# Optimization experiments

Hardware: AMD Instinct MI355X
Metric: run time of the kernel (lower is better)

Reference implementation:

```python
import jax, jax.numpy as jnp
import numpy as np

N = 50000     # nodes
E = 800000    # edges (before self-loops)
DIN = 128     # input feature dim
DH = 16       # per-head hidden dim (layer 1)
H = 8         # heads (layer 1)
DOUT = 64     # output classes (layer 2, heads=1)


def setup_inputs() -> dict:
    key = jax.random.key(0)
    ks = jax.random.split(key, 10)
    def rn(k, shape, scale=0.1):
        return jax.random.normal(k, shape, dtype=jnp.float32) * scale
    x = jax.random.normal(ks[0], (N, DIN), dtype=jnp.float32)
    edge_index = jax.random.randint(ks[1], (2, E), 0, N, dtype=jnp.int64)
    return {
        "x": x,
        "edge_index": edge_index,
        "W1": rn(ks[2], (DIN, H * DH)),
        "a_src1": rn(ks[3], (H, DH)),
        "a_dst1": rn(ks[4], (H, DH)),
        "b1": jnp.zeros((H * DH,), jnp.float32),
        "W2": rn(ks[5], (H * DH, DOUT)),
        "a_src2": rn(ks[6], (1, DOUT)),
        "a_dst2": rn(ks[7], (1, DOUT)),
        "b2": jnp.zeros((DOUT,), jnp.float32),
    }


def gat_conv(x, src, dst, W, a_src, a_dst, b, heads, out_dim):
    """PyG-style GATConv: edge attention + segment softmax over dst + scatter-add."""
    n = x.shape[0]
    h = (x @ W).reshape(n, heads, out_dim)                 # [N, H, D]
    alpha_src = jnp.sum(h * a_src, axis=-1)                # [N, H]
    alpha_dst = jnp.sum(h * a_dst, axis=-1)                # [N, H]
    e = jax.nn.leaky_relu(alpha_src[src] + alpha_dst[dst], 0.2)  # [Etot, H]
    # numerically-stable segment softmax grouped by destination node
    m = jax.ops.segment_max(e, dst, num_segments=n)        # [N, H]
    ex = jnp.exp(e - m[dst])
    s = jax.ops.segment_sum(ex, dst, num_segments=n)       # [N, H]
    alpha = ex / (s[dst] + 1e-16)                          # [Etot, H]
    msg = h[src] * alpha[..., None]                        # [Etot, H, D]
    out = jax.ops.segment_sum(msg, dst, num_segments=n)    # [N, H, D]
    return out.reshape(n, heads * out_dim) + b


def reference(x, W1, a_src1, a_dst1, b1, W2, a_src2, a_dst2, b2, edge_index):
    # eval mode: F.dropout(p=0.6, training=False) is identity
    loop = jnp.arange(N, dtype=edge_index.dtype)
    src = jnp.concatenate([edge_index[0], loop])  # add_self_loops=True (PyG default)
    dst = jnp.concatenate([edge_index[1], loop])
    h = gat_conv(x, src, dst, W1, a_src1, a_dst1, b1, H, DH)
    h = jax.nn.elu(h)
    h = gat_conv(h, src, dst, W2, a_src2, a_dst2, b2, 1, DOUT)
    return (h, jax.nn.log_softmax(h, axis=1))
```

## Files before the change

### kernel.cpp

```cpp
#include <hip/hip_runtime.h>

#define NN 50000
#define EE 800000
#define ET (EE + NN)

typedef unsigned short ushort_t;

__device__ __forceinline__ float bf2f(ushort_t u) {
    return __uint_as_float(((unsigned int)u) << 16);
}
__device__ __forceinline__ ushort_t f2bf(float f) {
    unsigned int u = __float_as_uint(f);
    u += 0x7fffu + ((u >> 16) & 1u);
    return (ushort_t)(u >> 16);
}
__device__ __forceinline__ float lrelu(float e) {
    return fmaxf(e, 0.f) + 0.2f * fminf(e, 0.f);
}
__device__ __forceinline__ float ldf(const void* p, int i, bool f32) {
    return f32 ? ((const float*)p)[i] : bf2f(((const ushort_t*)p)[i]);
}

__global__ __launch_bounds__(256) void sniff_kernel(const unsigned int* xw, const int* eiw, int* flags) {
    __shared__ int cnt0, cnt1;
    int t = threadIdx.x;
    if (t == 0) { cnt0 = 0; cnt1 = 0; }
    __syncthreads();
    float v = __uint_as_float(xw[t]);
    float a = fabsf(v);
    if ((a > 1e-6f && a < 1e6f) || v == 0.f) atomicAdd(&cnt0, 1);
    if (eiw[2 * t + 1] != 0) atomicAdd(&cnt1, 1);
    __syncthreads();
    if (t == 0) {
        flags[0] = (cnt0 >= 192) ? 1 : 0;
        flags[1] = (cnt1 <= 16) ? 1 : 0;
    }
}

__device__ __forceinline__ void edge_sd(const int* ei, int i, bool i64, int& s, int& d) {
    if (i < EE) {
        if (i64) { s = ei[2 * i]; d = ei[2 * (EE + i)]; }
        else     { s = ei[i];     d = ei[EE + i]; }
    } else {
        s = d = i - EE;
    }
}

__global__ __launch_bounds__(256) void degree_rank_kernel(const int* ei, int* deg, int* rank, const int* flags) {
    int i = blockIdx.x * 256 + threadIdx.x;
    if (i >= ET) return;
    bool i64 = flags[1] != 0;
    int s, d;
    edge_sd(ei, i, i64, s, d);
    rank[i] = atomicAdd(&deg[d], 1);
}

__global__ __launch_bounds__(1024) void scan_kernel(const int* deg, int* rowptr) {
    __shared__ int wsum[16];
    __shared__ int carry;
    if (threadIdx.x == 0) carry = 0;
    __syncthreads();
    int t = threadIdx.x;
    int lane = t & 63, wid = t >> 6;
    const int NI = NN / 4;
    for (int base = 0; base < NI; base += 1024) {
        int i4 = base + t;
        int4 dv = (i4 < NI) ? ((const int4*)deg)[i4] : make_int4(0, 0, 0, 0);
        int v = dv.x + dv.y + dv.z + dv.w;
        int x = v;
        #pragma unroll
        for (int off = 1; off < 64; off <<= 1) {
            int y = __shfl_up(x, off);
            if (lane >= off) x += y;
        }
        if (lane == 63) wsum[wid] = x;
        __syncthreads();
        if (t < 16) {
            int s = wsum[t];
            #pragma unroll
            for (int off = 1; off < 16; off <<= 1) {
                int y = __shfl_up(s, off);
                if (t >= off) s += y;
            }
            wsum[t] = s;
        }
        __syncthreads();
        int woff = ((wid > 0) ? wsum[wid - 1] : 0) + carry;
        int excl = x - v + woff;
        if (i4 < NI) {
            int e0 = excl, e1 = e0 + dv.x, e2 = e1 + dv.y, e3 = e2 + dv.z;
            ((int4*)rowptr)[i4] = make_int4(e0, e1, e2, e3);
        }
        int ct = wsum[15];
        __syncthreads();
        if (t == 0) carry += ct;
        __syncthreads();
    }
    if (threadIdx.x == 0) rowptr[NN] = carry;
}

__global__ __launch_bounds__(256) void fill_kernel(const int* ei, const int* rowptr, const int* rank,
                                                   int* col, const int* flags) {
    int i = blockIdx.x * 256 + threadIdx.x;
    if (i >= ET) return;
    bool i64 = flags[1] != 0;
    int s, d;
    edge_sd(ei, i, i64, s, d);
    col[rowptr[d] + rank[i]] = s;
}

#define FMA4(accv, wv, xs)                   \
    accv.x = fmaf(wv.x, xs, accv.x);         \
    accv.y = fmaf(wv.y, xs, accv.y);         \
    accv.z = fmaf(wv.z, xs, accv.z);         \
    accv.w = fmaf(wv.w, xs, accv.w);

template <bool AEXT, int NH>
__global__ __launch_bounds__(256) void gemm64_kernel(const void* Av, const void* Wv,
                                                     const void* a_src, const void* a_dst,
                                                     ushort_t* outb, float* asrc, float* adst,
                                                     int n, int wstride, int ostride,
                                                     const int* flags) {
    __shared__ __align__(16) float Wf[128 * 64];
    __shared__ __align__(16) float xT[128 * 64];
    bool f32 = flags[0] != 0;
    int t = threadIdx.x;
    int coloff = blockIdx.y * 64;

    if (f32) {
        const float* W = (const float*)Wv;
        for (int i = t; i < 2048; i += 256) {
            int k = i >> 4;
            int cp = i & 15;
            float4 wv = *(const float4*)(W + k * wstride + coloff + cp * 4);
            *(float4*)(&Wf[k * 64 + cp * 4]) = wv;
        }
    } else {
        const ushort_t* W = (const ushort_t*)Wv;
        for (int i = t; i < 4096; i += 256) {
            int k = i >> 5;
            int cp = i & 31;
            unsigned int v = *(const unsigned int*)(W + k * wstride + coloff + cp * 2);
            float2 w2 = make_float2(__uint_as_float(v << 16), __uint_as_float(v & 0xffff0000u));
            *(float2*)(&Wf[k * 64 + cp * 2]) = w2;
        }
    }

    int base = blockIdx.x * 64;
    int r = t & 63;
    int kc = t >> 6;
    int row = base + r;
    if (AEXT && !f32) {
        if (row < n) {
            const uint4* p = (const uint4*)((const ushort_t*)Av + (size_t)row * 128 + kc * 32);
            #pragma unroll
            for (int j = 0; j < 4; ++j) {
                uint4 q = p[j];
                int kb = kc * 32 + j * 8;
                xT[(kb + 0) * 64 + r] = __uint_as_float(q.x << 16);
                xT[(kb + 1) * 64 + r] = __uint_as_float(q.x & 0xffff0000u);
                xT[(kb + 2) * 64 + r] = __uint_as_float(q.y << 16);
                xT[(kb + 3) * 64 + r] = __uint_as_float(q.y & 0xffff0000u);
                xT[(kb + 4) * 64 + r] = __uint_as_float(q.z << 16);
                xT[(kb + 5) * 64 + r] = __uint_as_float(q.z & 0xffff0000u);
                xT[(kb + 6) * 64 + r] = __uint_as_float(q.w << 16);
                xT[(kb + 7) * 64 + r] = __uint_as_float(q.w & 0xffff0000u);
            }
        } else {
            #pragma unroll
            for (int j = 0; j < 32; ++j) xT[(kc * 32 + j) * 64 + r] = 0.f;
        }
    } else {
        if (row < n) {
            const float4* p = (const float4*)((const float*)Av + (size_t)row * 128 + kc * 32);
            #pragma unroll
            for (int j = 0; j < 8; ++j) {
                float4 q = p[j];
                int kb = kc * 32 + j * 4;
                xT[(kb + 0) * 64 + r] = q.x;
                xT[(kb + 1) * 64 + r] = q.y;
                xT[(kb + 2) * 64 + r] = q.z;
                xT[(kb + 3) * 64 + r] = q.w;
            }
        } else {
            #pragma unroll
            for (int j = 0; j < 32; ++j) xT[(kc * 32 + j) * 64 + r] = 0.f;
        }
    }
    __syncthreads();

    int cg = t & 15, rg = t >> 4;
    const float4* W4 = (const float4*)Wf;
    const float4* X4 = (const float4*)xT;
    float4 a0 = make_float4(0, 0, 0, 0), a1 = a0, a2 = a0, a3 = a0;
    #pragma unroll 4
    for (int k = 0; k < 128; ++k) {
        float4 wv = W4[k * 16 + cg];
        float4 xv = X4[k * 16 + rg];
        FMA4(a0, wv, xv.x)
        FMA4(a1, wv, xv.y)
        FMA4(a2, wv, xv.z)
        FMA4(a3, wv, xv.w)
    }

    int orow = base + rg * 4;
    int c0 = coloff + cg * 4;
    float4 av[4] = {a0, a1, a2, a3};
    #pragma unroll
    for (int j = 0; j < 4; ++j) {
        if (orow + j < n) {
            ushort4 o4;
            o4.x = f2bf(av[j].x); o4.y = f2bf(av[j].y);
            o4.z = f2bf(av[j].z); o4.w = f2bf(av[j].w);
            *(ushort4*)(outb + (size_t)(orow + j) * ostride + c0) = o4;
        }
    }

    float4 avs, avd;
    avs.x = ldf(a_src, c0 + 0, f32); avs.y = ldf(a_src, c0 + 1, f32);
    avs.z = ldf(a_src, c0 + 2, f32); avs.w = ldf(a_src, c0 + 3, f32);
    avd.x = ldf(a_dst, c0 + 0, f32); avd.y = ldf(a_dst, c0 + 1, f32);
    avd.z = ldf(a_dst, c0 + 2, f32); avd.w = ldf(a_dst, c0 + 3, f32);
    float ps[4], pd[4];
    #pragma unroll
    for (int j = 0; j < 4; ++j) {
        ps[j] = av[j].x * avs.x + av[j].y * avs.y + av[j].z * avs.z + av[j].w * avs.w;
        pd[j] = av[j].x * avd.x + av[j].y * avd.y + av[j].z * avd.z + av[j].w * avd.w;
    }
    const int span = (NH == 8) ? 4 : 16;
    #pragma unroll
    for (int stp = 1; stp < span; stp <<= 1) {
        #pragma unroll
        for (int j = 0; j < 4; ++j) {
            ps[j] += __shfl_xor(ps[j], stp);
            pd[j] += __shfl_xor(pd[j], stp);
        }
    }
    if ((cg & (span - 1)) == 0) {
        int hh = (NH == 8) ? (coloff / 16 + (cg >> 2)) : 0;
        #pragma unroll
        for (int j = 0; j < 4; ++j) {
            int rw = orow + j;
            if (rw < n) {
                asrc[(size_t)rw * NH + hh] = ps[j];
                adst[(size_t)rw * NH + hh] = pd[j];
            }
        }
    }
}

__global__ __launch_bounds__(256) void agg1_kernel(const int* rowptr, const int* col, const ushort_t* h1b,
                                                   const float* asrc, const float* adst,
                                                   const void* b1, float* hmid, const int* flags) {
    __shared__ float wle[4][8 * 72];
    __shared__ int lcol[4][64];
    bool f32 = flags[0] != 0;
    int lane = threadIdx.x & 63, wid = threadIdx.x >> 6;
    int d = blockIdx.x * 4 + wid;
    if (d >= NN) return;
    int start = rowptr[d], end = rowptr[d + 1];
    int hB = lane >> 3;
    const float4* dp = (const float4*)(adst + (size_t)d * 8);
    float4 ad0 = dp[0], ad1 = dp[1];
    float acc0 = 0.f, acc1 = 0.f, ssum = 0.f;
    for (int chunk = start; chunk < end; chunk += 64) {
        int cnt = min(64, end - chunk);
        int c = (chunk + lane < end) ? col[chunk + lane] : 0;
        lcol[wid][lane] = c;
        if (lane < cnt) {
            const float4* ap = (const float4*)(asrc + (size_t)c * 8);
            float4 s0 = ap[0], s1 = ap[1];
            wle[wid][0 * 72 + lane] = __expf(lrelu(s0.x + ad0.x));
            wle[wid][1 * 72 + lane] = __expf(lrelu(s0.y + ad0.y));
            wle[wid][2 * 72 + lane] = __expf(lrelu(s0.z + ad0.z));
            wle[wid][3 * 72 + lane] = __expf(lrelu(s0.w + ad0.w));
            wle[wid][4 * 72 + lane] = __expf(lrelu(s1.x + ad1.x));
            wle[wid][5 * 72 + lane] = __expf(lrelu(s1.y + ad1.y));
            wle[wid][6 * 72 + lane] = __expf(lrelu(s1.z + ad1.z));
            wle[wid][7 * 72 + lane] = __expf(lrelu(s1.w + ad1.w));
        }
        #pragma unroll 4
        for (int j = 0; j < cnt; ++j) {
            int s = lcol[wid][j];
            float ex = wle[wid][hB * 72 + j];
            unsigned int hv = *(const unsigned int*)(h1b + (size_t)s * 128 + lane * 2);
            ssum += ex;
            acc0 = fmaf(ex, __uint_as_float(hv << 16), acc0);
            acc1 = fmaf(ex, __uint_as_float(hv & 0xffff0000u), acc1);
        }
    }
    float inv = 1.f / (ssum + 1e-16f);
    float o0 = fmaf(acc0, inv, ldf(b1, lane * 2, f32));
    float o1 = fmaf(acc1, inv, ldf(b1, lane * 2 + 1, f32));
    o0 = (o0 > 0.f) ? o0 : (__expf(o0) - 1.f);
    o1 = (o1 > 0.f) ? o1 : (__expf(o1) - 1.f);
    *(float2*)(hmid + (size_t)d * 128 + lane * 2) = make_float2(o0, o1);
}

__global__ __launch_bounds__(256) void agg2_kernel(const int* rowptr, const int* col, const ushort_t* h2b,
                                                   const float* asrc, const float* adst,
                                                   const void* b2, float* out, const int* flags) {
    __shared__ float wle[4][64];
    __shared__ int lcol[4][64];
    bool f32 = flags[0] != 0;
    int lane = threadIdx.x & 63, wid = threadIdx.x >> 6;
    int d = blockIdx.x * 4 + wid;
    if (d >= NN) return;
    int start = rowptr[d], end = rowptr[d + 1];
    float ad = adst[d];
    float acc = 0.f, ssum = 0.f;
    for (int chunk = start; chunk < end; chunk += 64) {
        int cnt = min(64, end - chunk);
        int c = (chunk + lane < end) ? col[chunk + lane] : 0;
        lcol[wid][lane] = c;
        if (lane < cnt) wle[wid][lane] = __expf(lrelu(asrc[c] + ad));
        #pragma unroll 4
        for (int j = 0; j < cnt; ++j) {
            int s = lcol[wid][j];
            float ex = wle[wid][j];
            float hv = bf2f(h2b[(size_t)s * 64 + lane]);
            ssum += ex;
            acc = fmaf(ex, hv, acc);
        }
    }
    float o = acc / (ssum + 1e-16f) + ldf(b2, lane, f32);
    float mm = o;
    #pragma unroll
    for (int off = 1; off < 64; off <<= 1) mm = fmaxf(mm, __shfl_xor(mm, off));
    float texp = __expf(o - mm);
    float ts = texp;
    #pragma unroll
    for (int off = 1; off < 64; off <<= 1) ts += __shfl_xor(ts, off);
    float ls = o - mm - __logf(ts);
    out[(size_t)d * 64 + lane] = o;
    out[(size_t)NN * 64 + (size_t)d * 64 + lane] = ls;
}

extern "C" void kernel_launch(void* const* d_in, const int* in_sizes, int n_in,
                              void* d_out, int out_size, void* d_ws, size_t ws_size,
                              hipStream_t stream) {
    const void* x   = d_in[0];
    const int*  ei  = (const int*)d_in[1];
    const void* W1  = d_in[2];
    const void* as1 = d_in[3];
    const void* ad1 = d_in[4];
    const void* b1  = d_in[5];
    const void* W2  = d_in[6];
    const void* as2 = d_in[7];
    const void* ad2 = d_in[8];
    const void* b2  = d_in[9];
    float* out = (float*)d_out;

    char* w = (char*)d_ws;
    auto alloc = [&](size_t bytes) {
        void* p = (void*)w;
        w += (bytes + 255) & ~(size_t)255;
        return p;
    };
    int* flags    = (int*)alloc(256);
    int* deg      = (int*)alloc((size_t)NN * 4);
    int* rowptr   = (int*)alloc((size_t)(NN + 1) * 4);
    int* rank     = (int*)alloc((size_t)ET * 4);
    int* colx     = (int*)alloc((size_t)ET * 4);
    ushort_t* h1b = (ushort_t*)alloc((size_t)NN * 128 * 2);
    float* asrc1  = (float*)alloc((size_t)NN * 8 * 4);
    float* adst1  = (float*)alloc((size_t)NN * 8 * 4);
    float* hmid   = (float*)alloc((size_t)NN * 128 * 4);
    ushort_t* h2b = (ushort_t*)alloc((size_t)NN * 64 * 2);
    float* asrc2  = (float*)alloc((size_t)NN * 4);
    float* adst2  = (float*)alloc((size_t)NN * 4);

    sniff_kernel<<<1, 256, 0, stream>>>((const unsigned int*)x, ei, flags);

    hipMemsetAsync(deg, 0, (size_t)NN * 4, stream);
    degree_rank_kernel<<<(ET + 255) / 256, 256, 0, stream>>>(ei, deg, rank, flags);
    scan_kernel<<<1, 1024, 0, stream>>>(deg, rowptr);
    fill_kernel<<<(ET + 255) / 256, 256, 0, stream>>>(ei, rowptr, rank, colx, flags);

    dim3 g1((NN + 63) / 64, 2);
    gemm64_kernel<true, 8><<<g1, 256, 0, stream>>>(x, W1, as1, ad1, h1b, asrc1, adst1, NN, 128, 128, flags);
    agg1_kernel<<<(NN + 3) / 4, 256, 0, stream>>>(rowptr, colx, h1b, asrc1, adst1, b1, hmid, flags);

    dim3 g2((NN + 63) / 64, 1);
    gemm64_kernel<false, 1><<<g2, 256, 0, stream>>>((const void*)hmid, W2, as2, ad2, h2b, asrc2, adst2, NN, 64, 64, flags);
    agg2_kernel<<<(NN + 3) / 4, 256, 0, stream>>>(rowptr, colx, h2b, asrc2, adst2, b2, out, flags);
}
```

Baseline: 288.4 us.

## Privatize degree counters into eight copies and precompute byte offsets in aggregation

Degree counting now spreads atomics over eight private histogram copies chosen by block index, which is meant to cut atomic contention on hot destination counters. The single-block scan reads all eight copies, sums them, and writes per-copy start offsets back so the fill kernel can place edges directly. The aggregation kernels store precomputed byte offsets in shared memory and add __restrict__, which trims per-edge address arithmetic. The costs are eight times the memset and more memory traffic in the serial scan kernel.

New measurement: 312.3 us. 8.3% more time.

```diff
diff --git a/kernel.cpp b/kernel.cpp
--- a/kernel.cpp
+++ b/kernel.cpp
@@ -46,16 +46,17 @@
     }
 }
 
-__global__ __launch_bounds__(256) void degree_rank_kernel(const int* ei, int* deg, int* rank, const int* flags) {
+__global__ __launch_bounds__(256) void degree_rank_kernel(const int* ei, int* deg8, int* rank, const int* flags) {
     int i = blockIdx.x * 256 + threadIdx.x;
     if (i >= ET) return;
     bool i64 = flags[1] != 0;
+    int g = blockIdx.x & 7;
     int s, d;
     edge_sd(ei, i, i64, s, d);
-    rank[i] = atomicAdd(&deg[d], 1);
-}
-
-__global__ __launch_bounds__(1024) void scan_kernel(const int* deg, int* rowptr) {
+    rank[i] = atomicAdd(&deg8[(size_t)g * NN + d], 1);
+}
+
+__global__ __launch_bounds__(1024) void scan_kernel(int* deg8, int* rowptr) {
     __shared__ int wsum[16];
     __shared__ int carry;
     if (threadIdx.x == 0) carry = 0;
@@ -65,8 +66,18 @@
     const int NI = NN / 4;
     for (int base = 0; base < NI; base += 1024) {
         int i4 = base + t;
-        int4 dv = (i4 < NI) ? ((const int4*)deg)[i4] : make_int4(0, 0, 0, 0);
-        int v = dv.x + dv.y + dv.z + dv.w;
+        int4 dv[8];
+        int v = 0;
+        if (i4 < NI) {
+            #pragma unroll
+            for (int g = 0; g < 8; ++g) {
+                dv[g] = ((const int4*)(deg8 + (size_t)g * NN))[i4];
+                v += dv[g].x + dv[g].y + dv[g].z + dv[g].w;
+            }
+        } else {
+            #pragma unroll
+            for (int g = 0; g < 8; ++g) dv[g] = make_int4(0, 0, 0, 0);
+        }
         int x = v;
         #pragma unroll
         for (int off = 1; off < 64; off <<= 1) {
@@ -88,8 +99,22 @@
         int woff = ((wid > 0) ? wsum[wid - 1] : 0) + carry;
         int excl = x - v + woff;
         if (i4 < NI) {
-            int e0 = excl, e1 = e0 + dv.x, e2 = e1 + dv.y, e3 = e2 + dv.z;
-            ((int4*)rowptr)[i4] = make_int4(e0, e1, e2, e3);
+            int run = excl;
+            int4 ov[8];
+            int4 rp;
+            #pragma unroll
+            for (int j = 0; j < 4; ++j) {
+                (&rp.x)[j] = run;
+                #pragma unroll
+                for (int g = 0; g < 8; ++g) {
+                    (&ov[g].x)[j] = run;
+                    run += (&dv[g].x)[j];
+                }
+            }
+            ((int4*)rowptr)[i4] = rp;
+            #pragma unroll
+            for (int g = 0; g < 8; ++g)
+                ((int4*)(deg8 + (size_t)g * NN))[i4] = ov[g];
         }
         int ct = wsum[15];
         __syncthreads();
@@ -99,14 +124,15 @@
     if (threadIdx.x == 0) rowptr[NN] = carry;
 }
 
-__global__ __launch_bounds__(256) void fill_kernel(const int* ei, const int* rowptr, const int* rank,
+__global__ __launch_bounds__(256) void fill_kernel(const int* ei, const int* deg8off, const int* rank,
                                                    int* col, const int* flags) {
     int i = blockIdx.x * 256 + threadIdx.x;
     if (i >= ET) return;
     bool i64 = flags[1] != 0;
+    int g = blockIdx.x & 7;
     int s, d;
     edge_sd(ei, i, i64, s, d);
-    col[rowptr[d] + rank[i]] = s;
+    col[deg8off[(size_t)g * NN + d] + rank[i]] = s;
 }
 
 #define FMA4(accv, wv, xs)                   \
@@ -249,11 +275,12 @@
     }
 }
 
-__global__ __launch_bounds__(256) void agg1_kernel(const int* rowptr, const int* col, const ushort_t* h1b,
-                                                   const float* asrc, const float* adst,
-                                                   const void* b1, float* hmid, const int* flags) {
+__global__ __launch_bounds__(256) void agg1_kernel(const int* __restrict__ rowptr, const int* __restrict__ col,
+                                                   const ushort_t* __restrict__ h1b,
+                                                   const float* __restrict__ asrc, const float* __restrict__ adst,
+                                                   const void* b1, float* __restrict__ hmid, const int* flags) {
     __shared__ float wle[4][8 * 72];
-    __shared__ int lcol[4][64];
+    __shared__ int loff[4][64];
     bool f32 = flags[0] != 0;
     int lane = threadIdx.x & 63, wid = threadIdx.x >> 6;
     int d = blockIdx.x * 4 + wid;
@@ -262,11 +289,12 @@
     int hB = lane >> 3;
     const float4* dp = (const float4*)(adst + (size_t)d * 8);
     float4 ad0 = dp[0], ad1 = dp[1];
+    const char* hb = (const char*)h1b + lane * 4;
     float acc0 = 0.f, acc1 = 0.f, ssum = 0.f;
     for (int chunk = start; chunk < end; chunk += 64) {
         int cnt = min(64, end - chunk);
         int c = (chunk + lane < end) ? col[chunk + lane] : 0;
-        lcol[wid][lane] = c;
+        loff[wid][lane] = c << 8;
         if (lane < cnt) {
             const float4* ap = (const float4*)(asrc + (size_t)c * 8);
             float4 s0 = ap[0], s1 = ap[1];
@@ -281,9 +309,9 @@
         }
         #pragma unroll 4
         for (int j = 0; j < cnt; ++j) {
-            int s = lcol[wid][j];
+            int off = loff[wid][j];
             float ex = wle[wid][hB * 72 + j];
-            unsigned int hv = *(const unsigned int*)(h1b + (size_t)s * 128 + lane * 2);
+            unsigned int hv = *(const unsigned int*)(hb + off);
             ssum += ex;
             acc0 = fmaf(ex, __uint_as_float(hv << 16), acc0);
             acc1 = fmaf(ex, __uint_as_float(hv & 0xffff0000u), acc1);
@@ -297,28 +325,30 @@
     *(float2*)(hmid + (size_t)d * 128 + lane * 2) = make_float2(o0, o1);
 }
 
-__global__ __launch_bounds__(256) void agg2_kernel(const int* rowptr, const int* col, const ushort_t* h2b,
-                                                   const float* asrc, const float* adst,
-                                                   const void* b2, float* out, const int* flags) {
+__global__ __launch_bounds__(256) void agg2_kernel(const int* __restrict__ rowptr, const int* __restrict__ col,
+                                                   const ushort_t* __restrict__ h2b,
+                                                   const float* __restrict__ asrc, const float* __restrict__ adst,
+                                                   const void* b2, float* __restrict__ out, const int* flags) {
     __shared__ float wle[4][64];
-    __shared__ int lcol[4][64];
+    __shared__ int loff[4][64];
     bool f32 = flags[0] != 0;
     int lane = threadIdx.x & 63, wid = threadIdx.x >> 6;
     int d = blockIdx.x * 4 + wid;
     if (d >= NN) return;
     int start = rowptr[d], end = rowptr[d + 1];
     float ad = adst[d];
+    const char* hb = (const char*)h2b + lane * 2;
     float acc = 0.f, ssum = 0.f;
     for (int chunk = start; chunk < end; chunk += 64) {
         int cnt = min(64, end - chunk);
         int c = (chunk + lane < end) ? col[chunk + lane] : 0;
-        lcol[wid][lane] = c;
+        loff[wid][lane] = c << 7;
         if (lane < cnt) wle[wid][lane] = __expf(lrelu(asrc[c] + ad));
         #pragma unroll 4
         for (int j = 0; j < cnt; ++j) {
-            int s = lcol[wid][j];
+            int off = loff[wid][j];
             float ex = wle[wid][j];
-            float hv = bf2f(h2b[(size_t)s * 64 + lane]);
+            float hv = bf2f(*(const ushort_t*)(hb + off));
             ssum += ex;
             acc = fmaf(ex, hv, acc);
         }
@@ -358,7 +388,7 @@
         return p;
     };
     int* flags    = (int*)alloc(256);
-    int* deg      = (int*)alloc((size_t)NN * 4);
+    int* deg8     = (int*)alloc((size_t)8 * NN * 4);
     int* rowptr   = (int*)alloc((size_t)(NN + 1) * 4);
     int* rank     = (int*)alloc((size_t)ET * 4);
     int* colx     = (int*)alloc((size_t)ET * 4);
@@ -372,10 +402,10 @@
 
     sniff_kernel<<<1, 256, 0, stream>>>((const unsigned int*)x, ei, flags);
 
-    hipMemsetAsync(deg, 0, (size_t)NN * 4, stream);
-    degree_rank_kernel<<<(ET + 255) / 256, 256, 0, stream>>>(ei, deg, rank, flags);
-    scan_kernel<<<1, 1024, 0, stream>>>(deg, rowptr);
-    fill_kernel<<<(ET + 255) / 256, 256, 0, stream>>>(ei, rowptr, rank, colx, flags);
+    hipMemsetAsync(deg8, 0, (size_t)8 * NN * 4, stream);
+    degree_rank_kernel<<<(ET + 255) / 256, 256, 0, stream>>>(ei, deg8, rank, flags);
+    scan_kernel<<<1, 1024, 0, stream>>>(deg8, rowptr);
+    fill_kernel<<<(ET + 255) / 256, 256, 0, stream>>>(ei, deg8, rank, colx, flags);
 
     dim3 g1((NN + 63) / 64, 2);
     gemm64_kernel<true, 8><<<g1, 256, 0, stream>>>(x, W1, as1, ad1, h1b, asrc1, adst1, NN, 128, 128, flags);
```
